# Optimization experiments

Measured on AMD Instinct MI355X. Metric: run time of the kernel, lower is better.

The kernel has to match this reference:

```python
import jax, jax.numpy as jnp
import numpy as np

N_NODES, N_EDGES, N_GRAPHS = 20000, 320000, 8
IN_CH, OUT_CH = 16, 64


def gat_conv(x, src, dst, W, a_src, a_dst, bias, heads, ch, concat):
    # PyG-style GATConv: linear -> per-edge attention logits -> edge softmax over dst -> scatter-sum
    n = x.shape[0]
    h = (x @ W).reshape(n, heads, ch)                      # [N,H,C]
    alpha_src = jnp.einsum('nhc,hc->nh', h, a_src)          # [N,H]
    alpha_dst = jnp.einsum('nhc,hc->nh', h, a_dst)
    e = jax.nn.leaky_relu(alpha_src[src] + alpha_dst[dst], 0.2)  # [E,H]
    emax = jax.ops.segment_max(e, dst, num_segments=n)      # safe: self-loops guarantee coverage
    ee = jnp.exp(e - emax[dst])
    denom = jax.ops.segment_sum(ee, dst, num_segments=n)
    alpha = ee / denom[dst]                                 # [E,H]
    msg = h[src] * alpha[:, :, None]                        # [E,H,C]
    out = jax.ops.segment_sum(msg, dst, num_segments=n)     # [N,H,C]
    out = out.reshape(n, heads * ch) if concat else out.mean(axis=1)
    return out + bias


def setup_inputs() -> dict:
    key = jax.random.key(0)
    ks = jax.random.split(key, 32)
    d = {}
    d['x'] = jax.random.normal(ks[0], (N_NODES, IN_CH), dtype=jnp.float32)
    d['edge_index'] = jax.random.randint(ks[1], (2, N_EDGES), 0, N_NODES)
    d['function_idx'] = jax.random.randint(ks[2], (8000,), 0, N_NODES)
    d['flag'] = jnp.sort(jax.random.randint(ks[3], (8000,), 0, N_GRAPHS))
    d['decision_var_idxes'] = jax.random.randint(ks[4], (N_GRAPHS,), 0, N_NODES)
    s = 0.1
    # conv1: in 16 -> 8 heads x 8
    d['W1'] = jax.random.normal(ks[5], (IN_CH, 64)) * s
    d['a_src1'] = jax.random.normal(ks[6], (8, 8)) * s
    d['a_dst1'] = jax.random.normal(ks[7], (8, 8)) * s
    d['b1'] = jnp.zeros((64,), jnp.float32)
    # conv2, conv3: 64 -> 8 heads x 8
    d['W2'] = jax.random.normal(ks[8], (64, 64)) * s
    d['a_src2'] = jax.random.normal(ks[9], (8, 8)) * s
    d['a_dst2'] = jax.random.normal(ks[10], (8, 8)) * s
    d['b2'] = jnp.zeros((64,), jnp.float32)
    d['W3'] = jax.random.normal(ks[11], (64, 64)) * s
    d['a_src3'] = jax.random.normal(ks[12], (8, 8)) * s
    d['a_dst3'] = jax.random.normal(ks[13], (8, 8)) * s
    d['b3'] = jnp.zeros((64,), jnp.float32)
    # conv4: 64 -> 4 heads x 64, concat=False (mean over heads)
    d['W4'] = jax.random.normal(ks[14], (64, 4 * OUT_CH)) * s
    d['a_src4'] = jax.random.normal(ks[15], (4, OUT_CH)) * s
    d['a_dst4'] = jax.random.normal(ks[16], (4, OUT_CH)) * s
    d['b4'] = jnp.zeros((OUT_CH,), jnp.float32)
    d['Wp'] = jax.random.normal(ks[17], (OUT_CH, OUT_CH)) * s
    d['Wt'] = jax.random.normal(ks[18], (OUT_CH, OUT_CH)) * s
    d['Wo'] = jax.random.normal(ks[19], (2 * OUT_CH, 1)) * s
    d['bo'] = jnp.zeros((1,), jnp.float32)
    return d


def reference(x, edge_index, function_idx, flag, decision_var_idxes,
              W1, a_src1, a_dst1, b1, W2, a_src2, a_dst2, b2,
              W3, a_src3, a_dst3, b3, W4, a_src4, a_dst4, b4,
              Wp, Wt, Wo, bo):
    n = x.shape[0]
    loops = jnp.arange(n)
    src = jnp.concatenate([edge_index[0], loops])
    dst = jnp.concatenate([edge_index[1], loops])
    h = jax.nn.elu(gat_conv(x, src, dst, W1, a_src1, a_dst1, b1, 8, 8, True))
    h = jax.nn.elu(gat_conv(h, src, dst, W2, a_src2, a_dst2, b2, 8, 8, True))
    h = jax.nn.elu(gat_conv(h, src, dst, W3, a_src3, a_dst3, b3, 8, 8, True))
    h = jax.nn.elu(gat_conv(h, src, dst, W4, a_src4, a_dst4, b4, 4, OUT_CH, False))
    # per-graph sum-pool over function nodes
    fp = jax.ops.segment_sum(h[function_idx], flag, num_segments=N_GRAPHS)  # [B,64]
    fp = fp @ Wp
    tgt = h[decision_var_idxes] @ Wt                                        # [B,64]
    z = jax.nn.elu(jnp.concatenate([fp, tgt], axis=1))                      # [B,128]
    return z @ Wo + bo                                                      # [B,1]
```

## Files before the change

kernel.cpp:

```cpp
#include <hip/hip_runtime.h>
#include <hip/hip_bf16.h>
#include <math.h>

typedef __hip_bfloat16 bf16;
typedef unsigned short u16;
typedef __attribute__((ext_vector_type(8))) short bf16x8;
typedef __attribute__((ext_vector_type(4))) float f32x4;

#define DEG_CAP 96

__device__ __forceinline__ float b2f(bf16 v){ return __bfloat162float(v); }
__device__ __forceinline__ u16 f2bu(float f){
  bf16 h = __float2bfloat16(f);
  return *reinterpret_cast<u16*>(&h);
}
__device__ __forceinline__ float bu2f(u16 u){
  bf16 h = *reinterpret_cast<bf16*>(&u);
  return __bfloat162float(h);
}
__device__ __forceinline__ float eluf(float x){ return x > 0.f ? x : __expf(x) - 1.f; }
__device__ __forceinline__ float lrelu(float x){ return x > 0.f ? x : 0.2f * x; }
__device__ __forceinline__ float ldr(const void* p, int i, int f){
  return f ? ((const float*)p)[i] : b2f(((const bf16*)p)[i]);
}

#define DPP_F(x, ctrl) __int_as_float(__builtin_amdgcn_update_dpp(0, __float_as_int(x), (ctrl), 0xF, 0xF, true))
__device__ __forceinline__ float dpp_max8(float x){
  x = fmaxf(x, DPP_F(x, 0xB1));
  x = fmaxf(x, DPP_F(x, 0x4E));
  x = fmaxf(x, DPP_F(x, 0x141));
  return x;
}
__device__ __forceinline__ float dpp_sum8(float x){
  x += DPP_F(x, 0xB1);
  x += DPP_F(x, 0x4E);
  x += DPP_F(x, 0x141);
  return x;
}
__device__ __forceinline__ float dpp_max16(float x){
  x = fmaxf(x, DPP_F(x, 0xB1));
  x = fmaxf(x, DPP_F(x, 0x4E));
  x = fmaxf(x, DPP_F(x, 0x141));
  x = fmaxf(x, DPP_F(x, 0x140));
  return x;
}
__device__ __forceinline__ float dpp_sum16(float x){
  x += DPP_F(x, 0xB1);
  x += DPP_F(x, 0x4E);
  x += DPP_F(x, 0x141);
  x += DPP_F(x, 0x140);
  return x;
}
__device__ __forceinline__ float dpp_addx1(float x){ return x + DPP_F(x, 0xB1); }

__global__ void detect_zero_k(const u16* __restrict__ x, int nprobe, int* __restrict__ flag,
                              int* __restrict__ fill, float* __restrict__ fp, int n){
  int i = blockIdx.x * 256 + threadIdx.x;
  if (i < n) fill[i] = 0;
  if (i < 512) fp[i] = 0.f;
  if (blockIdx.x == 0){
    __shared__ int bad_s;
    if (threadIdx.x == 0) bad_s = 0;
    __syncthreads();
    int bad = 0;
    for (int k = threadIdx.x; k < nprobe; k += 256){
      int ex = (x[k] >> 7) & 0xFF;
      if (ex >= 0xC6) bad = 1;
    }
    if (bad) atomicOr(&bad_s, 1);
    __syncthreads();
    if (threadIdx.x == 0) *flag = bad_s;
  }
}

struct ConvDesc {
  const void* src[17];
  int off[18];
};

__global__ void prep_k(ConvDesc d, float* __restrict__ out, const int* __restrict__ flag,
                       int total, const int* __restrict__ ei, int E, int n,
                       int* __restrict__ fill, int* __restrict__ esrc,
                       const void* __restrict__ W4r, const void* __restrict__ as4r,
                       const void* __restrict__ ad4r, float* __restrict__ avs,
                       float* __restrict__ avd, u16* __restrict__ wzh,
                       u16* __restrict__ wzl,
                       const void* __restrict__ x_raw, const void* __restrict__ W1r,
                       const void* __restrict__ as1r, const void* __restrict__ ad1r,
                       u16* __restrict__ hl1, float* __restrict__ asrc1,
                       float* __restrict__ adst1,
                       int CB, int EB){
  __shared__ float wl1[16 * 64];
  __shared__ float xr1[16][20];
  int b = blockIdx.x;
  int f = *flag;
  int t = threadIdx.x;
  if (b < CB){
    int i = b * 256 + t;
    if (i >= total) return;
    int a = 0;
    while (i >= d.off[a + 1]) ++a;
    out[i] = ldr(d.src[a], i - d.off[a], f);
  } else if (b < CB + EB){
    int e = (b - CB) * 256 + t;
    if (e >= E + n) return;
    int s, dd;
    if (e < E){ s = ei[e]; dd = ei[E + e]; } else { s = e - E; dd = s; }
    int pos = atomicAdd(&fill[dd], 1);
    if (pos < DEG_CAP) esrc[dd * DEG_CAP + pos] = s;
  } else if (b < CB + EB + 64){
    int pb = b - CB - EB;
    int g = pb * 256 + t;
    int r = g >> 6, c = g & 63;
    int h = r >> 6, k = r & 63;
    float ww = 0.25f * ldr(W4r, k * 256 + h * 64 + c, f);
    u16 hi = f2bu(ww);
    wzh[c * 256 + r] = hi;
    wzl[c * 256 + r] = f2bu(ww - bu2f(hi));
    if (pb == 0){
      int th = t >> 6, tk = t & 63;
      float s1 = 0.f, s2 = 0.f;
      for (int cc = 0; cc < 64; ++cc){
        float w = ldr(W4r, tk * 256 + th * 64 + cc, f);
        s1 += w * ldr(as4r, th * 64 + cc, f);
        s2 += w * ldr(ad4r, th * 64 + cc, f);
      }
      avs[t] = s1;
      avd[t] = s2;
    }
  } else {
    int lb = b - CB - EB - 64;
    int base = lb * 16;
    int lane = t & 63, wv = t >> 6;
    int node = wv * 4 + (lane >> 4);
    int jj = lane & 15;
    for (int i = t; i < 1024; i += 256) wl1[i] = ldr(W1r, i, f);
    for (int q = t; q < 64; q += 256){
      int nd = q >> 2, k4 = q & 3;
      float4 v = make_float4(0.f, 0.f, 0.f, 0.f);
      if (base + nd < n){
        if (f){
          v = *(const float4*)((const float*)x_raw + (base + nd) * 16 + k4 * 4);
        } else {
          ushort4 v4 = *(const ushort4*)((const u16*)x_raw + (base + nd) * 16 + k4 * 4);
          v = make_float4(bu2f(v4.x), bu2f(v4.y), bu2f(v4.z), bu2f(v4.w));
        }
      }
      *(float4*)(&xr1[nd][k4 * 4]) = v;
    }
    __syncthreads();
    float ax = 0.f, ay = 0.f, az = 0.f, aw = 0.f;
#pragma unroll
    for (int k4 = 0; k4 < 4; ++k4){
      float4 xv = *(const float4*)(&xr1[node][k4 * 4]);
      float4 w0 = ((const float4*)wl1)[(k4 * 4 + 0) * 16 + jj];
      float4 w1 = ((const float4*)wl1)[(k4 * 4 + 1) * 16 + jj];
      float4 w2 = ((const float4*)wl1)[(k4 * 4 + 2) * 16 + jj];
      float4 w3 = ((const float4*)wl1)[(k4 * 4 + 3) * 16 + jj];
      ax += xv.x * w0.x + xv.y * w1.x + xv.z * w2.x + xv.w * w3.x;
      ay += xv.x * w0.y + xv.y * w1.y + xv.z * w2.y + xv.w * w3.y;
      az += xv.x * w0.z + xv.y * w1.z + xv.z * w2.z + xv.w * w3.z;
      aw += xv.x * w0.w + xv.y * w1.w + xv.z * w2.w + xv.w * w3.w;
    }
    int gn = base + node;
    if (gn < n){
      ushort4 o4;
      o4.x = f2bu(ax); o4.y = f2bu(ay); o4.z = f2bu(az); o4.w = f2bu(aw);
      ((ushort4*)(hl1 + gn * 64))[jj] = o4;
    }
    float as_[4], ad_[4];
#pragma unroll
    for (int c = 0; c < 4; ++c){
      as_[c] = ldr(as1r, 4 * jj + c, f);
      ad_[c] = ldr(ad1r, 4 * jj + c, f);
    }
    float s1 = ax * as_[0] + ay * as_[1] + az * as_[2] + aw * as_[3];
    float s2 = ax * ad_[0] + ay * ad_[1] + az * ad_[2] + aw * ad_[3];
    s1 = dpp_addx1(s1);
    s2 = dpp_addx1(s2);
    if (gn < n){
      int hh = jj >> 1;
      if ((jj & 1) == 0) asrc1[gn * 8 + hh] = s1;
      else               adst1[gn * 8 + hh] = s2;
    }
  }
}

template<int NEXT>
__global__ void agg8f_k(const u16* __restrict__ hlin, const float* __restrict__ asrc,
                        const float* __restrict__ adst, const int* __restrict__ cnts,
                        const int* __restrict__ esrc, const float* __restrict__ bias,
                        const float* __restrict__ Wn,
                        const float* __restrict__ a_srcn, const float* __restrict__ a_dstn,
                        const float* __restrict__ avs, const float* __restrict__ avd,
                        u16* __restrict__ hout, u16* __restrict__ ylin,
                        float* __restrict__ asrco, float* __restrict__ adsto, int n){
  __shared__ float wl[NEXT == 1 ? 4096 : 1];
  __shared__ float os[4][64];
  if (NEXT == 1){
    for (int q = threadIdx.x; q < 1024; q += 256)
      ((float4*)wl)[q] = ((const float4*)Wn)[q];
    __syncthreads();
  }
  int node = (blockIdx.x * blockDim.x + threadIdx.x) >> 6;
  if (node >= n) return;
  int lane = threadIdx.x & 63;
  int wv = (threadIdx.x >> 6) & 3;
  int h = lane >> 3;
  int j = lane & 7;
  int cp = lane & 15;
  int q  = lane >> 4;
  int hh = cp >> 1;
  int wlane0 = hh * 8 + q;
  int wlane1 = hh * 8 + 4 + q;
  int sclane = hh * 8;
  int beg = node * DEG_CAP;
  int cnt = cnts[node]; if (cnt > DEG_CAP) cnt = DEG_CAP;
  int end = beg + cnt;
  float ad = adst[node * 8 + h];

  float m = -INFINITY, swp = 0.f;
  float4 acc = make_float4(0.f, 0.f, 0.f, 0.f);

  int   s_cur = 0; float l_cur = -INFINITY;
  if (beg + j < end){ s_cur = esrc[beg + j]; l_cur = lrelu(asrc[s_cur * 8 + h] + ad); }
  int s0c = __shfl(s_cur, q), s1c = __shfl(s_cur, 4 + q);
  ushort4 hv0 = *(const ushort4*)(hlin + s0c * 64 + cp * 4);
  ushort4 hv1 = *(const ushort4*)(hlin + s1c * 64 + cp * 4);
  int   s_nx = 0; float l_nx = -INFINITY;
  if (beg + 8 + j < end){ s_nx = esrc[beg + 8 + j]; l_nx = lrelu(asrc[s_nx * 8 + h] + ad); }

  for (int b0 = beg; b0 < end; b0 += 8){
    int s0n = __shfl(s_nx, q), s1n = __shfl(s_nx, 4 + q);
    ushort4 hv0n = *(const ushort4*)(hlin + s0n * 64 + cp * 4);
    ushort4 hv1n = *(const ushort4*)(hlin + s1n * 64 + cp * 4);
    int p2 = b0 + 16 + j;
    int s_n2 = 0; float l_n2 = -INFINITY;
    if (p2 < end){ s_n2 = esrc[p2]; l_n2 = lrelu(asrc[s_n2 * 8 + h] + ad); }
    float bm = dpp_max8(l_cur);
    float mn = fmaxf(m, bm);
    if (!__all(bm <= m)){
      float scale = __expf(m - mn);
      swp *= scale;
      float scale_g = __shfl(scale, sclane);
      acc.x *= scale_g; acc.y *= scale_g; acc.z *= scale_g; acc.w *= scale_g;
      m = mn;
    }
    float w = (b0 + j < end) ? __expf(l_cur - m) : 0.f;
    swp += w;
    float w0 = __shfl(w, wlane0);
    float w1 = __shfl(w, wlane1);
    acc.x += bu2f(hv0.x) * w0 + bu2f(hv1.x) * w1;
    acc.y += bu2f(hv0.y) * w0 + bu2f(hv1.y) * w1;
    acc.z += bu2f(hv0.z) * w0 + bu2f(hv1.z) * w1;
    acc.w += bu2f(hv0.w) * w0 + bu2f(hv1.w) * w1;
    hv0 = hv0n; hv1 = hv1n;
    l_cur = l_nx;
    s_nx = s_n2; l_nx = l_n2;
  }
  acc.x += __shfl_xor(acc.x, 16); acc.x += __shfl_xor(acc.x, 32);
  acc.y += __shfl_xor(acc.y, 16); acc.y += __shfl_xor(acc.y, 32);
  acc.z += __shfl_xor(acc.z, 16); acc.z += __shfl_xor(acc.z, 32);
  acc.w += __shfl_xor(acc.w, 16); acc.w += __shfl_xor(acc.w, 32);
  swp = dpp_sum8(swp);
  float sw_g = __shfl(swp, sclane);
  float4 bv = ((const float4*)bias)[cp];
  float4 o4;
  o4.x = eluf(acc.x / sw_g + bv.x);
  o4.y = eluf(acc.y / sw_g + bv.y);
  o4.z = eluf(acc.z / sw_g + bv.z);
  o4.w = eluf(acc.w / sw_g + bv.w);

  if (NEXT == 1){
    if (lane < 16) *(float4*)(&os[wv][cp * 4]) = o4;
    int jj = lane & 15, kk = lane >> 4;
    const float4* osr = (const float4*)(&os[wv][kk * 16]);
    float ax = 0.f, ay = 0.f, az = 0.f, aw = 0.f;
#pragma unroll
    for (int k4 = 0; k4 < 4; ++k4){
      float4 xv = osr[k4];
      float4 w0 = ((const float4*)wl)[(kk * 16 + k4 * 4 + 0) * 16 + jj];
      float4 w1 = ((const float4*)wl)[(kk * 16 + k4 * 4 + 1) * 16 + jj];
      float4 w2 = ((const float4*)wl)[(kk * 16 + k4 * 4 + 2) * 16 + jj];
      float4 w3 = ((const float4*)wl)[(kk * 16 + k4 * 4 + 3) * 16 + jj];
      ax += xv.x * w0.x + xv.y * w1.x + xv.z * w2.x + xv.w * w3.x;
      ay += xv.x * w0.y + xv.y * w1.y + xv.z * w2.y + xv.w * w3.y;
      az += xv.x * w0.z + xv.y * w1.z + xv.z * w2.z + xv.w * w3.z;
      aw += xv.x * w0.w + xv.y * w1.w + xv.z * w2.w + xv.w * w3.w;
    }
    ax += __shfl_xor(ax, 16); ax += __shfl_xor(ax, 32);
    ay += __shfl_xor(ay, 16); ay += __shfl_xor(ay, 32);
    az += __shfl_xor(az, 16); az += __shfl_xor(az, 32);
    aw += __shfl_xor(aw, 16); aw += __shfl_xor(aw, 32);
    if (lane < 16){
      ushort4 y4;
      y4.x = f2bu(ax); y4.y = f2bu(ay); y4.z = f2bu(az); y4.w = f2bu(aw);
      ((ushort4*)(ylin + node * 64))[jj] = y4;
      float4 as = *(const float4*)(a_srcn + 4 * jj);
      float4 adn = *(const float4*)(a_dstn + 4 * jj);
      float s1 = ax * as.x + ay * as.y + az * as.z + aw * as.w;
      float s2 = ax * adn.x + ay * adn.y + az * adn.z + aw * adn.w;
      s1 = dpp_addx1(s1);
      s2 = dpp_addx1(s2);
      int nh = jj >> 1;
      if ((jj & 1) == 0) asrco[node * 8 + nh] = s1;
      else               adsto[node * 8 + nh] = s2;
    }
  } else {
    if (lane < 16){
      ushort4 ho;
      ho.x = f2bu(o4.x); ho.y = f2bu(o4.y); ho.z = f2bu(o4.z); ho.w = f2bu(o4.w);
      ((ushort4*)(hout + node * 64))[cp] = ho;
      *(float4*)(&os[wv][cp * 4]) = o4;
    }
    int t8 = lane & 7, ah = (lane >> 3) & 3, sd = lane >> 5;
    const float* av = sd ? avd : avs;
    const float4* op = (const float4*)(&os[wv][t8 * 8]);
    const float4* ap = (const float4*)(av + ah * 64 + t8 * 8);
    float4 o0 = op[0], o1 = op[1];
    float4 a0 = ap[0], a1 = ap[1];
    float part = o0.x * a0.x + o0.y * a0.y + o0.z * a0.z + o0.w * a0.w
               + o1.x * a1.x + o1.y * a1.y + o1.z * a1.z + o1.w * a1.w;
    part = dpp_sum8(part);
    if (t8 == 0){
      if (sd == 0) asrco[node * 4 + ah] = part;
      else         adsto[node * 4 + ah] = part;
    }
  }
}

__global__ void aggz_k(const u16* __restrict__ h3, const float* __restrict__ asrc,
                       const float* __restrict__ adst, const int* __restrict__ cnts,
                       const int* __restrict__ esrc, const int* __restrict__ fidx,
                       const int* __restrict__ dec, u16* __restrict__ zc,
                       int lm, int m){
  int li = (blockIdx.x * blockDim.x + threadIdx.x) >> 6;
  if (li >= lm) return;
  int node = (li < m) ? fidx[li] : dec[li - m];
  int lane = threadIdx.x & 63;
  int h = lane >> 4, j = lane & 15;
  int beg = node * DEG_CAP;
  int cnt = cnts[node]; if (cnt > DEG_CAP) cnt = DEG_CAP;
  int end = beg + cnt;
  float4 adv = *(const float4*)(adst + node * 4);
  float adh = h == 0 ? adv.x : h == 1 ? adv.y : h == 2 ? adv.z : adv.w;

  float m_ = -INFINITY, swp = 0.f;
  float acc[4][4] = {{0.f, 0.f, 0.f, 0.f}, {0.f, 0.f, 0.f, 0.f},
                     {0.f, 0.f, 0.f, 0.f}, {0.f, 0.f, 0.f, 0.f}};
  int   s_nx = 0; float l_nx = -INFINITY;
  if (beg + j < end){ s_nx = esrc[beg + j]; l_nx = lrelu(asrc[s_nx * 4 + h] + adh); }
  for (int b0 = beg; b0 < end; b0 += 16){
    int s = s_nx; float l = l_nx;
    int p2 = b0 + 16 + j;
    s_nx = 0; l_nx = -INFINITY;
    if (p2 < end){ s_nx = esrc[p2]; l_nx = lrelu(asrc[s_nx * 4 + h] + adh); }
    float bm = dpp_max16(l);
    float mn = fmaxf(m_, bm);
    if (!__all(bm <= m_)){
      float scale = __expf(m_ - mn);
      swp *= scale;
      float sc0 = __shfl(scale, 0),  sc1 = __shfl(scale, 16);
      float sc2 = __shfl(scale, 32), sc3 = __shfl(scale, 48);
#pragma unroll
      for (int c = 0; c < 4; ++c){
        acc[0][c] *= sc0; acc[1][c] *= sc1; acc[2][c] *= sc2; acc[3][c] *= sc3;
      }
      m_ = mn;
    }
    float w = (b0 + j < end) ? __expf(l - m_) : 0.f;
    swp += w;
#pragma unroll
    for (int e4 = 0; e4 < 4; ++e4){
      int sl = e4 * 4 + h;
      int se = __shfl(s, sl);
      float w0 = __shfl(w, sl);
      float w1 = __shfl(w, 16 + sl);
      float w2 = __shfl(w, 32 + sl);
      float w3 = __shfl(w, 48 + sl);
      ushort4 hv = *(const ushort4*)(h3 + (size_t)se * 64 + j * 4);
      float x0 = bu2f(hv.x), x1 = bu2f(hv.y), x2 = bu2f(hv.z), x3 = bu2f(hv.w);
      acc[0][0] += x0 * w0; acc[0][1] += x1 * w0; acc[0][2] += x2 * w0; acc[0][3] += x3 * w0;
      acc[1][0] += x0 * w1; acc[1][1] += x1 * w1; acc[1][2] += x2 * w1; acc[1][3] += x3 * w1;
      acc[2][0] += x0 * w2; acc[2][1] += x1 * w2; acc[2][2] += x2 * w2; acc[2][3] += x3 * w2;
      acc[3][0] += x0 * w3; acc[3][1] += x1 * w3; acc[3][2] += x2 * w3; acc[3][3] += x3 * w3;
    }
  }
  swp = dpp_sum16(swp);
#pragma unroll
  for (int hh = 0; hh < 4; ++hh){
#pragma unroll
    for (int c = 0; c < 4; ++c){
      acc[hh][c] += __shfl_xor(acc[hh][c], 16);
      acc[hh][c] += __shfl_xor(acc[hh][c], 32);
    }
  }
  float swh = __shfl(swp, h * 16);
  float inv = 1.f / swh;
#pragma unroll
  for (int hh = 0; hh < 4; ++hh){
    if (h == hh){
      ushort4 o;
      o.x = f2bu(acc[hh][0] * inv); o.y = f2bu(acc[hh][1] * inv);
      o.z = f2bu(acc[hh][2] * inv); o.w = f2bu(acc[hh][3] * inv);
      ((ushort4*)(zc + (size_t)li * 256))[hh * 16 + j] = o;
    }
  }
}

__global__ void linear4_pool_k(const u16* __restrict__ Z, const u16* __restrict__ Wh,
                               const u16* __restrict__ Wl, const float* __restrict__ bias,
                               const int* __restrict__ flag_arr, float* __restrict__ fp,
                               u16* __restrict__ h4tail, int lm, int m){
  __shared__ float accs[512];
  int t = threadIdx.x;
  int base = blockIdx.x * 64;
  if (base >= lm) return;
  for (int i = t; i < 512; i += 256) accs[i] = 0.f;
  __syncthreads();
  int lane = t & 63;
  int wv = t >> 6;
  int wbase = base + wv * 16;
  int r16 = lane & 15, kg = lane >> 4;
  if (wbase < lm){
    int row = wbase + r16;
    int rowc = row < lm ? row : lm - 1;
    const u16* zp = Z + (size_t)rowc * 256 + kg * 8;
    const u16* wh = Wh + r16 * 256 + kg * 8;
    const u16* wlp = Wl + r16 * 256 + kg * 8;
    f32x4 ac[4] = {{0.f, 0.f, 0.f, 0.f}, {0.f, 0.f, 0.f, 0.f},
                   {0.f, 0.f, 0.f, 0.f}, {0.f, 0.f, 0.f, 0.f}};
#pragma unroll
    for (int k0 = 0; k0 < 256; k0 += 32){
      bf16x8 a = *(const bf16x8*)(zp + k0);
#pragma unroll
      for (int ct = 0; ct < 4; ++ct){
        bf16x8 bh = *(const bf16x8*)(wh + ct * 4096 + k0);
        ac[ct] = __builtin_amdgcn_mfma_f32_16x16x32_bf16(a, bh, ac[ct], 0, 0, 0);
      }
#pragma unroll
      for (int ct = 0; ct < 4; ++ct){
        bf16x8 bl = *(const bf16x8*)(wlp + ct * 4096 + k0);
        ac[ct] = __builtin_amdgcn_mfma_f32_16x16x32_bf16(a, bl, ac[ct], 0, 0, 0);
      }
    }
    int r0 = wbase + kg * 4;
#pragma unroll
    for (int i = 0; i < 4; ++i){
      int r = r0 + i;
      if (r >= lm) break;
      int g = (r < m) ? flag_arr[r] : -1;
#pragma unroll
      for (int ct = 0; ct < 4; ++ct){
        int jj = ct * 16 + r16;
        float v = eluf(ac[ct][i] + bias[jj]);
        if (g >= 0) atomicAdd(&accs[g * 64 + jj], v);
        else        h4tail[(size_t)(r - m) * 64 + jj] = f2bu(v);
      }
    }
  }
  __syncthreads();
  int rbeg = base, rend = base + 64;
  if (rend > m) rend = m;
  if (rbeg < rend){
    int gmin = flag_arr[rbeg], gmax = flag_arr[rend - 1];
    int cnt = (gmax - gmin + 1) * 64;
    for (int i = t; i < cnt; i += 256){
      float v = accs[gmin * 64 + i];
      if (v != 0.f) atomicAdd(&fp[gmin * 64 + i], v);
    }
  }
}

__global__ void final_k(const float* __restrict__ fp, const u16* __restrict__ h4tail,
                        const float* __restrict__ Wp, const float* __restrict__ Wt,
                        const float* __restrict__ Wo, const float* __restrict__ bo,
                        void* __restrict__ out, const int* __restrict__ dflag){
  __shared__ float fps[512];
  int t = threadIdx.x;
  fps[t] = fp[t];
  __syncthreads();
  int g = t >> 6;
  int j = t & 63;
  const u16* tr = h4tail + (size_t)g * 64;
  float a = 0.f, b = 0.f;
  for (int k = 0; k < 64; ++k){
    a += fps[g * 64 + k] * Wp[k * 64 + j];
    b += bu2f(tr[k]) * Wt[k * 64 + j];
  }
  float v = eluf(a) * Wo[j] + eluf(b) * Wo[64 + j];
  for (int off = 32; off > 0; off >>= 1) v += __shfl_down(v, off);
  if (j == 0){
    float r = v + bo[0];
    if (*dflag) ((float*)out)[g] = r;
    else        ((bf16*)out)[g] = __float2bfloat16(r);
  }
}


extern "C" void kernel_launch(void* const* d_in, const int* in_sizes, int n_in,
                              void* d_out, int out_size, void* d_ws, size_t ws_size,
                              hipStream_t stream) {
  const int*  ei    = (const int*)d_in[1];
  const int*  fidx  = (const int*)d_in[2];
  const int*  flagg = (const int*)d_in[3];
  const int*  dec   = (const int*)d_in[4];

  const int N = in_sizes[0] / 16;
  const int E = in_sizes[1] / 2;
  const int M = in_sizes[2];
  const int NG = in_sizes[4];
  const int LM = M + NG;
  const int ET = E + N;

  const int fidxs[17] = {5,6,7,8,9,10,11,12,13,14,15,16,20,21,22,23,24};
  ConvDesc cd;
  int tot = 0;
  for (int k = 0; k < 17; ++k){
    cd.src[k] = d_in[fidxs[k]];
    cd.off[k] = tot;
    tot += in_sizes[fidxs[k]];
  }
  cd.off[17] = tot;

  char* p = (char*)d_ws;
  auto carve = [&](size_t bytes) -> void* {
    void* r = (void*)p;
    p += (bytes + 255) & ~(size_t)255;
    return r;
  };
  int*   dflag   = (int*)carve(4);
  float* conv    = (float*)carve((size_t)tot * 4);
  u16*   hlA     = (u16*)carve((size_t)N * 64 * 2);
  u16*   hlB     = (u16*)carve((size_t)N * 64 * 2);
  u16*   h3buf   = (u16*)carve((size_t)N * 64 * 2);
  u16*   zbuf    = (u16*)carve((size_t)LM * 256 * 2);
  u16*   h4tail  = (u16*)carve((size_t)NG * 64 * 2);
  float* asrcA   = (float*)carve((size_t)N * 8 * 4);
  float* adstA   = (float*)carve((size_t)N * 8 * 4);
  float* asrcB   = (float*)carve((size_t)N * 8 * 4);
  float* adstB   = (float*)carve((size_t)N * 8 * 4);
  int*   fill    = (int*)carve((size_t)N * 4);
  int*   esrc    = (int*)carve((size_t)N * DEG_CAP * 4);
  float* fp      = (float*)carve(8 * 64 * 4);
  float* avs     = (float*)carve(256 * 4);
  float* avd     = (float*)carve(256 * 4);
  u16*   wzh     = (u16*)carve(16384 * 2);
  u16*   wzl     = (u16*)carve(16384 * 2);

  if ((size_t)(p - (char*)d_ws) > ws_size) return;

  const float* cas2 = conv + cd.off[5],  *cad2 = conv + cd.off[6],  *cb1 = conv + cd.off[3];
  const float* cW2 = conv + cd.off[4],   *cb2 = conv + cd.off[7];
  const float* cW3 = conv + cd.off[8],  *cas3 = conv + cd.off[9],  *cad3 = conv + cd.off[10], *cb3 = conv + cd.off[11];
  const float* cb4 = conv + cd.off[12];
  const float* cWp = conv + cd.off[13], *cWt = conv + cd.off[14], *cWo = conv + cd.off[15], *cbo = conv + cd.off[16];

  const int TB = 256;
  int nprobe = in_sizes[0] < 4096 ? in_sizes[0] : 4096;
  int zb_blocks = (N + 255) / 256;
  int CB = (tot + 255) / 256;
  int EB = (ET + 255) / 256;
  int ls_blocks = (N + 15) / 16;

  detect_zero_k<<<zb_blocks, TB, 0, stream>>>((const u16*)d_in[0], nprobe, dflag, fill, fp, N);
  prep_k<<<CB + EB + 64 + ls_blocks, TB, 0, stream>>>(
      cd, conv, dflag, tot, ei, E, N, fill, esrc,
      d_in[17], d_in[18], d_in[19], avs, avd, wzh, wzl,
      d_in[0], d_in[5], d_in[6], d_in[7], hlA, asrcA, adstA, CB, EB);

  int agg_blocks = (N * 64 + TB - 1) / TB;
  int aggz_blocks = (LM * 64 + TB - 1) / TB;
  int mf_blocks  = (LM + 63) / 64;

  agg8f_k<1><<<agg_blocks, TB, 0, stream>>>(hlA, asrcA, adstA, fill, esrc, cb1,
                                            cW2, cas2, cad2, nullptr, nullptr,
                                            nullptr, hlB, asrcB, adstB, N);
  agg8f_k<1><<<agg_blocks, TB, 0, stream>>>(hlB, asrcB, adstB, fill, esrc, cb2,
                                            cW3, cas3, cad3, nullptr, nullptr,
                                            nullptr, hlA, asrcA, adstA, N);
  agg8f_k<2><<<agg_blocks, TB, 0, stream>>>(hlA, asrcA, adstA, fill, esrc, cb3,
                                            nullptr, nullptr, nullptr, avs, avd,
                                            h3buf, nullptr, asrcB, adstB, N);
  aggz_k<<<aggz_blocks, TB, 0, stream>>>(h3buf, asrcB, adstB, fill, esrc,
                                         fidx, dec, zbuf, LM, M);
  linear4_pool_k<<<mf_blocks, TB, 0, stream>>>(zbuf, wzh, wzl, cb4, flagg, fp,
                                               h4tail, LM, M);
  final_k<<<1, 512, 0, stream>>>(fp, h4tail, cWp, cWt, cWo, cbo, d_out, dflag);
}
```

Measured before the change: 231.7 us.

## Fuse layer-4 aggregation with linear projection and graph pooling in one kernel

Merges the per-node layer-4 attention aggregation and the MFMA linear/ELU/pool kernel into a single 512-thread kernel. Each block aggregates 8 nodes into shared memory, then one wave runs the MFMA projection over those rows. This removes the global Z buffer round trip and one kernel launch. In exchange, the MFMA tiles are half-used (only 8 of 16 rows are valid), the other 7 waves sit idle during the matmul, and the weights are re-read per block of 8 rows, with more blocks issuing fp atomics.

```diff
diff --git a/kernel.cpp b/kernel.cpp
--- a/kernel.cpp
+++ b/kernel.cpp
@@ -329,22 +329,35 @@
   }
 }
 
-__global__ void aggz_k(const u16* __restrict__ h3, const float* __restrict__ asrc,
-                       const float* __restrict__ adst, const int* __restrict__ cnts,
-                       const int* __restrict__ esrc, const int* __restrict__ fidx,
-                       const int* __restrict__ dec, u16* __restrict__ zc,
-                       int lm, int m){
-  int li = (blockIdx.x * blockDim.x + threadIdx.x) >> 6;
-  if (li >= lm) return;
-  int node = (li < m) ? fidx[li] : dec[li - m];
-  int lane = threadIdx.x & 63;
+__global__ void aggz4p_k(const u16* __restrict__ h3, const float* __restrict__ asrc,
+                         const float* __restrict__ adst, const int* __restrict__ cnts,
+                         const int* __restrict__ esrc, const int* __restrict__ fidx,
+                         const int* __restrict__ dec,
+                         const u16* __restrict__ Wh, const u16* __restrict__ Wl,
+                         const float* __restrict__ bias,
+                         const int* __restrict__ flag_arr, float* __restrict__ fp,
+                         u16* __restrict__ h4tail, int lm, int m){
+  __shared__ u16 zs[8 * 264];
+  __shared__ float accs[512];
+  int t = threadIdx.x;
+  int wv = t >> 6;
+  int lane = t & 63;
+  int base = blockIdx.x * 8;
+  int li = base + wv;
+  accs[t] = 0.f;
+
+  bool alive = (li < lm);
+  int node = 0;
+  if (alive) node = (li < m) ? fidx[li] : dec[li - m];
   int h = lane >> 4, j = lane & 15;
   int beg = node * DEG_CAP;
-  int cnt = cnts[node]; if (cnt > DEG_CAP) cnt = DEG_CAP;
+  int cnt = alive ? cnts[node] : 0; if (cnt > DEG_CAP) cnt = DEG_CAP;
   int end = beg + cnt;
-  float4 adv = *(const float4*)(adst + node * 4);
-  float adh = h == 0 ? adv.x : h == 1 ? adv.y : h == 2 ? adv.z : adv.w;
-
+  float adh = 0.f;
+  if (alive){
+    float4 adv = *(const float4*)(adst + node * 4);
+    adh = h == 0 ? adv.x : h == 1 ? adv.y : h == 2 ? adv.z : adv.w;
+  }
   float m_ = -INFINITY, swp = 0.f;
   float acc[4][4] = {{0.f, 0.f, 0.f, 0.f}, {0.f, 0.f, 0.f, 0.f},
                      {0.f, 0.f, 0.f, 0.f}, {0.f, 0.f, 0.f, 0.f}};
@@ -395,37 +408,24 @@
       acc[hh][c] += __shfl_xor(acc[hh][c], 32);
     }
   }
-  float swh = __shfl(swp, h * 16);
-  float inv = 1.f / swh;
-#pragma unroll
-  for (int hh = 0; hh < 4; ++hh){
-    if (h == hh){
-      ushort4 o;
-      o.x = f2bu(acc[hh][0] * inv); o.y = f2bu(acc[hh][1] * inv);
-      o.z = f2bu(acc[hh][2] * inv); o.w = f2bu(acc[hh][3] * inv);
-      ((ushort4*)(zc + (size_t)li * 256))[hh * 16 + j] = o;
-    }
-  }
-}
-
-__global__ void linear4_pool_k(const u16* __restrict__ Z, const u16* __restrict__ Wh,
-                               const u16* __restrict__ Wl, const float* __restrict__ bias,
-                               const int* __restrict__ flag_arr, float* __restrict__ fp,
-                               u16* __restrict__ h4tail, int lm, int m){
-  __shared__ float accs[512];
-  int t = threadIdx.x;
-  int base = blockIdx.x * 64;
-  if (base >= lm) return;
-  for (int i = t; i < 512; i += 256) accs[i] = 0.f;
+  if (alive){
+    float swh = __shfl(swp, h * 16);
+    float inv = 1.f / swh;
+#pragma unroll
+    for (int hh = 0; hh < 4; ++hh){
+      if (h == hh){
+        ushort4 o;
+        o.x = f2bu(acc[hh][0] * inv); o.y = f2bu(acc[hh][1] * inv);
+        o.z = f2bu(acc[hh][2] * inv); o.w = f2bu(acc[hh][3] * inv);
+        ((ushort4*)(zs + wv * 264))[hh * 16 + j] = o;
+      }
+    }
+  }
   __syncthreads();
-  int lane = t & 63;
-  int wv = t >> 6;
-  int wbase = base + wv * 16;
-  int r16 = lane & 15, kg = lane >> 4;
-  if (wbase < lm){
-    int row = wbase + r16;
-    int rowc = row < lm ? row : lm - 1;
-    const u16* zp = Z + (size_t)rowc * 256 + kg * 8;
+
+  if (wv == 0){
+    int r16 = lane & 15, kg = lane >> 4;
+    const u16* zp = zs + (r16 & 7) * 264 + kg * 8;
     const u16* wh = Wh + r16 * 256 + kg * 8;
     const u16* wlp = Wl + r16 * 256 + kg * 8;
     f32x4 ac[4] = {{0.f, 0.f, 0.f, 0.f}, {0.f, 0.f, 0.f, 0.f},
@@ -444,10 +444,11 @@
         ac[ct] = __builtin_amdgcn_mfma_f32_16x16x32_bf16(a, bl, ac[ct], 0, 0, 0);
       }
     }
-    int r0 = wbase + kg * 4;
 #pragma unroll
     for (int i = 0; i < 4; ++i){
-      int r = r0 + i;
+      int rl = kg * 4 + i;
+      if (rl >= 8) break;
+      int r = base + rl;
       if (r >= lm) break;
       int g = (r < m) ? flag_arr[r] : -1;
 #pragma unroll
@@ -460,12 +461,11 @@
     }
   }
   __syncthreads();
-  int rbeg = base, rend = base + 64;
-  if (rend > m) rend = m;
-  if (rbeg < rend){
-    int gmin = flag_arr[rbeg], gmax = flag_arr[rend - 1];
-    int cnt = (gmax - gmin + 1) * 64;
-    for (int i = t; i < cnt; i += 256){
+  int rend = base + 8; if (rend > m) rend = m;
+  if (base < rend){
+    int gmin = flag_arr[base], gmax = flag_arr[rend - 1];
+    int cntf = (gmax - gmin + 1) * 64;
+    for (int i = t; i < cntf; i += 512){
       float v = accs[gmin * 64 + i];
       if (v != 0.f) atomicAdd(&fp[gmin * 64 + i], v);
     }
@@ -534,7 +534,6 @@
   u16*   hlA     = (u16*)carve((size_t)N * 64 * 2);
   u16*   hlB     = (u16*)carve((size_t)N * 64 * 2);
   u16*   h3buf   = (u16*)carve((size_t)N * 64 * 2);
-  u16*   zbuf    = (u16*)carve((size_t)LM * 256 * 2);
   u16*   h4tail  = (u16*)carve((size_t)NG * 64 * 2);
   float* asrcA   = (float*)carve((size_t)N * 8 * 4);
   float* adstA   = (float*)carve((size_t)N * 8 * 4);
@@ -570,8 +569,7 @@
       d_in[0], d_in[5], d_in[6], d_in[7], hlA, asrcA, adstA, CB, EB);
 
   int agg_blocks = (N * 64 + TB - 1) / TB;
-  int aggz_blocks = (LM * 64 + TB - 1) / TB;
-  int mf_blocks  = (LM + 63) / 64;
+  int az_blocks  = (LM + 7) / 8;
 
   agg8f_k<1><<<agg_blocks, TB, 0, stream>>>(hlA, asrcA, adstA, fill, esrc, cb1,
                                             cW2, cas2, cad2, nullptr, nullptr,
@@ -582,9 +580,8 @@
   agg8f_k<2><<<agg_blocks, TB, 0, stream>>>(hlA, asrcA, adstA, fill, esrc, cb3,
                                             nullptr, nullptr, nullptr, avs, avd,
                                             h3buf, nullptr, asrcB, adstB, N);
-  aggz_k<<<aggz_blocks, TB, 0, stream>>>(h3buf, asrcB, adstB, fill, esrc,
-                                         fidx, dec, zbuf, LM, M);
-  linear4_pool_k<<<mf_blocks, TB, 0, stream>>>(zbuf, wzh, wzl, cb4, flagg, fp,
-                                               h4tail, LM, M);
+  aggz4p_k<<<az_blocks, 512, 0, stream>>>(h3buf, asrcB, adstB, fill, esrc,
+                                          fidx, dec, wzh, wzl, cb4, flagg, fp,
+                                          h4tail, LM, M);
   final_k<<<1, 512, 0, stream>>>(fp, h4tail, cWp, cWt, cWo, cbo, d_out, dflag);
 }
```

Measured after the change: 228.9 us (median of 2 runs). Within noise of the previous version (-1.2%).
